# Performance work log

Measured on AMD Instinct MI355X. Metric: run time of the kernel, lower is better.

Reference implementation:

```python
import jax, jax.numpy as jnp
import numpy as np

B, T, H = 64, 256, 768
INIT = 0.05  # keras 'uniform' initializer range


def setup_inputs() -> dict:
    key = jax.random.key(0)
    ks = jax.random.split(key, 11)
    u = lambda k, shape: jax.random.uniform(k, shape, jnp.float32, -INIT, INIT)
    return {
        "q": jax.random.normal(ks[0], (B, T, H), jnp.float32),
        "p": jax.random.normal(ks[1], (B, T, H), jnp.float32),
        "Wc1": u(ks[2], (H, T)),
        "Wc2": u(ks[3], (H, T)),
        "vc": u(ks[4], (T, 1)),
        "Wb": u(ks[5], (H, H)),
        "Wd": u(ks[6], (H, 1)),
        "vd": u(ks[7], (T, 1)),
        "Wm": u(ks[8], (H, 1)),
        "vm": u(ks[9], (T, 1)),
    }


def reference(q, p, Wc1, Wc2, vc, Wb, Wd, vd, Wm, vm):
    # --- additive (concat-style) attention ---
    whq = q @ Wc1                      # [B,T,T]
    whp = p @ Wc2                      # [B,T,T]
    # vc (T,1) broadcasts along axis -2 (the p index i)
    sc = jnp.tanh(whp + jnp.swapaxes(whq, 1, 2)) * vc
    qc = jax.nn.softmax(sc, axis=-1) @ q             # [B,T,H]

    # --- bilinear attention ---
    sb = (p @ Wb) @ jnp.swapaxes(q, 1, 2)            # [B,T,T]
    qb = jax.nn.softmax(sb, axis=-1) @ q

    # --- elementwise-product attention ---
    # sum_h q[b,j,h]*p[b,i,h]*Wd[h]  ==  (p * Wd^T) @ q^T, avoids [B,T,T,H]
    sd_raw = jnp.einsum('bih,bjh->bij', p * Wd[:, 0], q)
    sd = jnp.tanh(sd_raw) * vd[:, 0]                 # vd broadcasts along q index j
    qd = jax.nn.softmax(sd, axis=-1) @ q

    # --- elementwise-difference attention ---
    # sum_h (q[b,j,h]-p[b,i,h])*Wm[h] == (q@Wm)[b,j] - (p@Wm)[b,i]
    qWm = (q @ Wm)[:, :, 0]                          # [B,T]
    pWm = (p @ Wm)[:, :, 0]                          # [B,T]
    sm = jnp.tanh(qWm[:, None, :] - pWm[:, :, None]) * vm[:, 0]
    qm = jax.nn.softmax(sm, axis=-1) @ q

    return (qc, qb, qd, qm)
```

## Files before the change

### kernel.cpp

```cpp
#include <hip/hip_runtime.h>
#include <hip/hip_bf16.h>
#include <stdint.h>

#define NB 64
#define NT 256
#define NH 768

typedef float f32x4 __attribute__((ext_vector_type(4)));
typedef __bf16 bf16x8 __attribute__((ext_vector_type(8)));

static __device__ __forceinline__ uint16_t f2bf(float f) {
  union { float f; uint32_t u; } v; v.f = f;
  uint32_t r = v.u + 0x7FFFu + ((v.u >> 16) & 1u);
  return (uint16_t)(r >> 16);
}
static __device__ __forceinline__ float bf2f(uint16_t h) {
  union { uint32_t u; float f; } v; v.u = ((uint32_t)h) << 16;
  return v.f;
}

typedef const __attribute__((address_space(1))) uint32_t* gp1_t;
typedef __attribute__((address_space(3))) uint32_t* lp3_t;
static __device__ __forceinline__ void gload_lds16(const uint16_t* g, uint16_t* l) {
  __builtin_amdgcn_global_load_lds((gp1_t)g, (lp3_t)l, 16, 0, 0);
}

static __device__ __forceinline__ int xcd_flat(int nwg) {
  int lin = (int)blockIdx.x;
  return (lin & 7) * (nwg >> 3) + (lin >> 3);
}

#define SLOT_U16 16384

static __device__ __forceinline__ void stage_part(
    const uint16_t* __restrict__ Ap, const uint16_t* __restrict__ Bp,
    int k0, int lda, int ldb, int part, uint16_t* __restrict__ slot,
    int wid, int lane) {
  const int isB = part >> 1;
  const int row = (part & 1) * 128 + wid * 16 + (lane >> 2);
  const int kcol = ((lane & 3) * 8) ^ (((lane >> 5) & 1) << 4);
  const uint16_t* src = isB ? Bp + (long)row * ldb + (k0 + kcol)
                            : Ap + (long)row * lda + (k0 + kcol);
  gload_lds16(src, slot + part * 4096 + wid * 512);
}

template <int NPROD, int NKPER>
static __device__ __forceinline__ void gemm256_core(
    const uint16_t* __restrict__ A0, const uint16_t* __restrict__ A1,
    const uint16_t* __restrict__ A2,
    const uint16_t* __restrict__ B0, const uint16_t* __restrict__ B1,
    const uint16_t* __restrict__ B2,
    int lda, int ldb, uint16_t* __restrict__ lds, f32x4 acc[8][4]) {
  const int tid = (int)threadIdx.x;
  const int wid = tid >> 6, lane = tid & 63;
  const int r = lane & 15, quad = lane >> 4;
  const int wm = wid >> 2, wn = wid & 3;
  const int ks = (quad * 8) ^ ((r >> 3) << 4);
  const int abase = (wm * 128 + r) * 32 + ks;
  const int bbase = 8192 + (wn * 64 + r) * 32 + ks;
  constexpr int nk = NPROD * NKPER;

#define TILE_AB(t, Ap, Bp, k0)                                      \
  {                                                                 \
    int pr_ = 0, kk_ = (t);                                         \
    if (NPROD > 1) { pr_ = (t) / NKPER; kk_ = (t) - pr_ * NKPER; }  \
    Ap = pr_ == 0 ? A0 : (pr_ == 1 ? A1 : A2);                      \
    Bp = pr_ == 0 ? B0 : (pr_ == 1 ? B1 : B2);                      \
    k0 = kk_ * 32;                                                  \
  }

  {
    const uint16_t* Ap; const uint16_t* Bp; int k0;
    TILE_AB(0, Ap, Bp, k0);
#pragma unroll
    for (int s = 0; s < 4; ++s) stage_part(Ap, Bp, k0, lda, ldb, s, lds, wid, lane);
    TILE_AB(1, Ap, Bp, k0);
#pragma unroll
    for (int s = 0; s < 4; ++s) stage_part(Ap, Bp, k0, lda, ldb, s, lds + SLOT_U16, wid, lane);
  }

  int slot = 0;
  for (int kt = 0; kt < nk; ++kt) {
    uint16_t* cur = lds + slot * SLOT_U16;
    int ns = slot + 2; if (ns >= 3) ns -= 3;
    uint16_t* nxt = lds + ns * SLOT_U16;
    const uint16_t* An = A0; const uint16_t* Bn = B0; int k0n = 0;
    const bool more2 = (kt + 2 < nk), more1 = (kt + 1 < nk);
    if (more2) TILE_AB(kt + 2, An, Bn, k0n);

#pragma unroll
    for (int p = 0; p < 4; ++p) {
      if (more2) stage_part(An, Bn, k0n, lda, ldb, p, nxt, wid, lane);
      if (p == 0) {
        if (more2)      asm volatile("s_waitcnt vmcnt(5)" ::: "memory");
        else if (more1) asm volatile("s_waitcnt vmcnt(4)" ::: "memory");
        else            asm volatile("s_waitcnt vmcnt(0)" ::: "memory");
        __builtin_amdgcn_s_barrier();
      }
      const int mg = p >> 1, ng = p & 1;
      bf16x8 av[4]; bf16x8 bv[2];
#pragma unroll
      for (int i = 0; i < 4; ++i)
        av[i] = *(const bf16x8*)&cur[abase + (mg * 4 + i) * 512];
#pragma unroll
      for (int j = 0; j < 2; ++j)
        bv[j] = *(const bf16x8*)&cur[bbase + (ng * 2 + j) * 512];
      if (p == 3) {
        asm volatile("s_waitcnt lgkmcnt(0)" ::: "memory");
        __builtin_amdgcn_s_barrier();
      }
      __builtin_amdgcn_s_setprio(1);
#pragma unroll
      for (int i = 0; i < 4; ++i)
#pragma unroll
        for (int j = 0; j < 2; ++j)
          acc[mg * 4 + i][ng * 2 + j] = __builtin_amdgcn_mfma_f32_16x16x32_bf16(
              av[i], bv[j], acc[mg * 4 + i][ng * 2 + j], 0, 0, 0);
      __builtin_amdgcn_s_setprio(0);
    }
    ++slot; if (slot == 3) slot = 0;
  }
#undef TILE_AB
}

static __device__ __forceinline__ void acc_zero8(f32x4 acc[8][4]) {
#pragma unroll
  for (int i = 0; i < 8; ++i)
#pragma unroll
    for (int j = 0; j < 4; ++j) acc[i][j] = (f32x4){0.f, 0.f, 0.f, 0.f};
}

static __device__ __forceinline__ void epi256_f32(const f32x4 acc[8][4],
                                                  float* __restrict__ C, int ldc) {
  const int lane = (int)threadIdx.x & 63, wid = (int)threadIdx.x >> 6;
  const int r = lane & 15, quad = lane >> 4;
  const int wm = wid >> 2, wn = wid & 3;
#pragma unroll
  for (int mi = 0; mi < 8; ++mi) {
    long row = wm * 128 + mi * 16 + quad * 4;
#pragma unroll
    for (int ni = 0; ni < 4; ++ni) {
      long col = wn * 64 + ni * 16 + r;
#pragma unroll
      for (int t = 0; t < 4; ++t) C[(row + t) * ldc + col] = acc[mi][ni][t];
    }
  }
}

static __device__ __forceinline__ void epi256_bf16(const f32x4 acc[8][4],
                                                   uint16_t* __restrict__ C, int ldc) {
  const int lane = (int)threadIdx.x & 63, wid = (int)threadIdx.x >> 6;
  const int r = lane & 15, quad = lane >> 4;
  const int wm = wid >> 2, wn = wid & 3;
#pragma unroll
  for (int mi = 0; mi < 8; ++mi) {
    long row = wm * 128 + mi * 16 + quad * 4;
#pragma unroll
    for (int ni = 0; ni < 4; ++ni) {
      long col = wn * 64 + ni * 16 + r;
#pragma unroll
      for (int t = 0; t < 4; ++t) C[(row + t) * ldc + col] = f2bf(acc[mi][ni][t]);
    }
  }
}

static __device__ __forceinline__ void epi256_split(const f32x4 acc[8][4],
                                                    uint16_t* __restrict__ Ch,
                                                    uint16_t* __restrict__ Cl, int ldc) {
  const int lane = (int)threadIdx.x & 63, wid = (int)threadIdx.x >> 6;
  const int r = lane & 15, quad = lane >> 4;
  const int wm = wid >> 2, wn = wid & 3;
#pragma unroll
  for (int mi = 0; mi < 8; ++mi) {
    long row = wm * 128 + mi * 16 + quad * 4;
#pragma unroll
    for (int ni = 0; ni < 4; ++ni) {
      long col = wn * 64 + ni * 16 + r;
#pragma unroll
      for (int t = 0; t < 4; ++t) {
        float v = acc[mi][ni][t];
        uint16_t hi = f2bf(v);
        Ch[(row + t) * ldc + col] = hi;
        Cl[(row + t) * ldc + col] = f2bf(v - bf2f(hi));
      }
    }
  }
}

__global__ __launch_bounds__(256) void prep_all(
    const float* __restrict__ q, const float* __restrict__ p,
    const float* __restrict__ Wc1, const float* __restrict__ Wc2,
    const float* __restrict__ Wb, const float* __restrict__ Wd,
    const float* __restrict__ Wm,
    uint16_t* __restrict__ q_hi, uint16_t* __restrict__ q_lo,
    uint16_t* __restrict__ p_hi, uint16_t* __restrict__ p_lo,
    uint16_t* __restrict__ pd, uint16_t* __restrict__ qT,
    uint16_t* __restrict__ Wc1T, uint16_t* __restrict__ Wc2T,
    uint16_t* __restrict__ WbTh, uint16_t* __restrict__ WbTl,
    float* __restrict__ qWm, float* __restrict__ pWm) {
  __shared__ float smem[32 * 33];
  const int blk = (int)blockIdx.x;
  const int tid = (int)threadIdx.x;
  if (blk < NB * NT) {
    const long base = (long)blk * NH;
    float sq = 0.f, sp = 0.f;
#pragma unroll
    for (int k = 0; k < 3; ++k) {
      int h = tid + 256 * k;
      long idx = base + h;
      float qv = q[idx], pv = p[idx];
      uint16_t qh = f2bf(qv);
      q_hi[idx] = qh; q_lo[idx] = f2bf(qv - bf2f(qh));
      uint16_t ph = f2bf(pv);
      p_hi[idx] = ph; p_lo[idx] = f2bf(pv - bf2f(ph));
      pd[idx] = f2bf(pv * Wd[h]);
      float w = Wm[h];
      sq += qv * w; sp += pv * w;
    }
    for (int o = 32; o; o >>= 1) { sq += __shfl_down(sq, o); sp += __shfl_down(sp, o); }
    int lane = tid & 63, wv = tid >> 6;
    if (lane == 0) { smem[wv] = sq; smem[4 + wv] = sp; }
    __syncthreads();
    if (tid == 0) {
      qWm[blk] = smem[0] + smem[1] + smem[2] + smem[3];
      pWm[blk] = smem[4] + smem[5] + smem[6] + smem[7];
    }
  } else if (blk < NB * NT + 24 * 8 * NB) {
    int t = blk - NB * NT;
    int ht = t % 24, tt = (t / 24) % 8, b = t / 192;
    int h0 = ht * 32, t0 = tt * 32;
    int tx = tid & 31, ty = tid >> 5;
    const float* src = q + ((long)b * NT + t0) * NH + h0;
    for (int s = 0; s < 32; s += 8) smem[(ty + s) * 33 + tx] = src[(long)(ty + s) * NH + tx];
    __syncthreads();
    uint16_t* dst = qT + ((long)b * NH + h0) * NT + t0;
    for (int s = 0; s < 32; s += 8) dst[(long)(ty + s) * NT + tx] = f2bf(smem[tx * 33 + ty + s]);
  } else {
    int idx = (blk - (NB * NT + 24 * 8 * NB)) * 256 + tid;
    if (idx < NT * NH) {
      int i = idx / NH, h = idx % NH;
      Wc1T[idx] = f2bf(Wc1[h * NT + i]);
      Wc2T[idx] = f2bf(Wc2[h * NT + i]);
    }
    if (idx < NH * NH) {
      int n = idx / NH, k = idx % NH;
      float w = Wb[k * NH + n];
      uint16_t hi = f2bf(w);
      WbTh[idx] = hi;
      WbTl[idx] = f2bf(w - bf2f(hi));
    }
  }
}

__global__ __launch_bounds__(512, 2) void gemm_big3(
    const uint16_t* __restrict__ Wc1T, const uint16_t* __restrict__ Wc2T,
    const uint16_t* __restrict__ q_hi, const uint16_t* __restrict__ p_hi,
    const uint16_t* __restrict__ p_lo, const uint16_t* __restrict__ pd,
    const uint16_t* __restrict__ WbTh, const uint16_t* __restrict__ WbTl,
    uint16_t* __restrict__ whqT, uint16_t* __restrict__ whp,
    uint16_t* __restrict__ sd,
    uint16_t* __restrict__ pWbh, uint16_t* __restrict__ pWbl) {
  __shared__ __align__(16) uint16_t lds[3 * SLOT_U16];
  const long sQP = (long)NT * NH, sTT = (long)NT * NT;
  int w = xcd_flat(384);
  f32x4 acc[8][4];
  acc_zero8(acc);
  if (w < 192) {
    const int b = w / 3, op = w - b * 3;
    const uint16_t* A; const uint16_t* B; uint16_t* C;
    if (op == 0)      { A = Wc1T;           B = q_hi + b * sQP; C = whqT + b * sTT; }
    else if (op == 1) { A = p_hi + b * sQP; B = Wc2T;           C = whp  + b * sTT; }
    else              { A = pd   + b * sQP; B = q_hi + b * sQP; C = sd   + b * sTT; }
    gemm256_core<1, 24>(A, nullptr, nullptr, B, nullptr, nullptr, NH, NH, lds, acc);
    epi256_bf16(acc, C, NT);
  } else {
    const int w2 = w - 192;
    const int b = w2 / 3, nt = w2 - b * 3;
    const uint16_t* Ah = p_hi + b * sQP;
    const uint16_t* Al = p_lo + b * sQP;
    const uint16_t* Bh = WbTh + (long)nt * 256 * NH;
    const uint16_t* Bl = WbTl + (long)nt * 256 * NH;
    gemm256_core<3, 24>(Ah, Ah, Al, Bh, Bl, Bh, NH, NH, lds, acc);
    epi256_split(acc, pWbh + b * sQP + nt * 256, pWbl + b * sQP + nt * 256, NH);
  }
}

__global__ __launch_bounds__(512, 2) void gemm_sb(
    const uint16_t* __restrict__ pWbh, const uint16_t* __restrict__ pWbl,
    const uint16_t* __restrict__ q_hi, const uint16_t* __restrict__ q_lo,
    float* __restrict__ sb0, float* __restrict__ sb1, float* __restrict__ sb2) {
  __shared__ __align__(16) uint16_t lds[3 * SLOT_U16];
  const long sQP = (long)NT * NH, sTT = (long)NT * NT;
  int w = xcd_flat(192);
  const int b = w / 3, pr = w - b * 3;
  const uint16_t* A = (pr == 2 ? pWbl : pWbh) + b * sQP;
  const uint16_t* B = (pr == 1 ? q_lo : q_hi) + b * sQP;
  float* C = (pr == 0 ? sb0 : (pr == 1 ? sb1 : sb2)) + b * sTT;
  f32x4 acc[8][4];
  acc_zero8(acc);
  gemm256_core<1, 24>(A, nullptr, nullptr, B, nullptr, nullptr, NH, NH, lds, acc);
  epi256_f32(acc, C, NT);
}

__global__ __launch_bounds__(512, 2) void gemm_pv(
    const uint16_t* __restrict__ P, const uint16_t* __restrict__ qT,
    float* __restrict__ out) {
  __shared__ __align__(16) uint16_t lds[3 * SLOT_U16];
  const long sQP = (long)NT * NH, sTT = (long)NT * NT;
  const long PB = (long)NB * sTT, nqp = (long)NB * sQP;
  int w = xcd_flat(768);
  const int b = w / 12, rem = w - b * 12;
  const int a = rem >> 2 == 0 ? 0 : rem / 3, nt = rem - (rem / 3) * 3;
  const uint16_t* A = P + (long)(rem / 3) * PB + b * sTT;
  const uint16_t* B = qT + b * sQP + (long)nt * 256 * NT;
  f32x4 acc[8][4];
  acc_zero8(acc);
  gemm256_core<1, 8>(A, nullptr, nullptr, B, nullptr, nullptr, NT, NT, lds, acc);
  (void)a;
  epi256_f32(acc, out + (long)(rem / 3) * nqp + b * sQP + (long)nt * 256, NH);
}

__global__ __launch_bounds__(64) void softmax_k(
    const uint16_t* __restrict__ whp, const uint16_t* __restrict__ whqT,
    const float* __restrict__ sb0, const float* __restrict__ sb1,
    const float* __restrict__ sb2, const uint16_t* __restrict__ sd,
    const float* __restrict__ qWm, const float* __restrict__ pWm,
    const float* __restrict__ vc, const float* __restrict__ vd,
    const float* __restrict__ vm,
    uint16_t* __restrict__ P) {
  int bi = blockIdx.x;
  int b = bi >> 8, i = bi & 255;
  int lane = threadIdx.x;
  long rowoff = (long)bi * NT;
  const long PB = (long)NB * NT * NT;
  float vci = vc[i];
  float pwm = pWm[(long)b * NT + i];
  float vals[4][4];
#pragma unroll
  for (int u = 0; u < 4; ++u) {
    int j = lane + 64 * u;
    long off = rowoff + j;
    vals[0][u] = tanhf(bf2f(whp[off]) + bf2f(whqT[off])) * vci;
    vals[1][u] = sb0[off] + sb1[off] + sb2[off];
    vals[2][u] = tanhf(bf2f(sd[off])) * vd[j];
    vals[3][u] = tanhf(qWm[(long)b * NT + j] - pwm) * vm[j];
  }
#pragma unroll
  for (int a = 0; a < 4; ++a) {
    float m = fmaxf(fmaxf(vals[a][0], vals[a][1]), fmaxf(vals[a][2], vals[a][3]));
    for (int o = 32; o; o >>= 1) m = fmaxf(m, __shfl_xor(m, o));
    float e[4], s = 0.f;
#pragma unroll
    for (int u = 0; u < 4; ++u) { e[u] = __expf(vals[a][u] - m); s += e[u]; }
    for (int o = 32; o; o >>= 1) s += __shfl_xor(s, o);
    float inv = 1.f / s;
#pragma unroll
    for (int u = 0; u < 4; ++u)
      P[a * PB + rowoff + lane + 64 * u] = f2bf(e[u] * inv);
  }
}

extern "C" void kernel_launch(void* const* d_in, const int* in_sizes, int n_in,
                              void* d_out, int out_size, void* d_ws, size_t ws_size,
                              hipStream_t stream) {
  const float* q   = (const float*)d_in[0];
  const float* p   = (const float*)d_in[1];
  const float* Wc1 = (const float*)d_in[2];
  const float* Wc2 = (const float*)d_in[3];
  const float* vc  = (const float*)d_in[4];
  const float* Wb  = (const float*)d_in[5];
  const float* Wd  = (const float*)d_in[6];
  const float* vd  = (const float*)d_in[7];
  const float* Wm  = (const float*)d_in[8];
  const float* vm  = (const float*)d_in[9];
  (void)in_sizes; (void)n_in; (void)out_size; (void)ws_size;

  char* ws = (char*)d_ws;
  size_t o = 0;
  auto alloc = [&](size_t bytes) -> char* {
    char* r = ws + o;
    o = (o + bytes + 255) & ~(size_t)255;
    return r;
  };
  const size_t nqp = (size_t)NB * NT * NH;
  const size_t ntt = (size_t)NB * NT * NT;

  uint16_t* Wc1T = (uint16_t*)alloc((size_t)NT * NH * 2);
  uint16_t* Wc2T = (uint16_t*)alloc((size_t)NT * NH * 2);
  uint16_t* WbTh = (uint16_t*)alloc((size_t)NH * NH * 2);
  uint16_t* WbTl = (uint16_t*)alloc((size_t)NH * NH * 2);
  uint16_t* q_hi = (uint16_t*)alloc(nqp * 2);
  uint16_t* q_lo = (uint16_t*)alloc(nqp * 2);
  uint16_t* p_hi = (uint16_t*)alloc(nqp * 2);
  uint16_t* p_lo = (uint16_t*)alloc(nqp * 2);
  uint16_t* pd   = (uint16_t*)alloc(nqp * 2);
  uint16_t* qT   = (uint16_t*)alloc(nqp * 2);
  float*    qWmB = (float*)alloc((size_t)NB * NT * 4);
  float*    pWmB = (float*)alloc((size_t)NB * NT * 4);
  uint16_t* whp  = (uint16_t*)alloc(ntt * 2);
  uint16_t* whqT = (uint16_t*)alloc(ntt * 2);
  uint16_t* pWbh = (uint16_t*)alloc(nqp * 2);
  uint16_t* pWbl = (uint16_t*)alloc(nqp * 2);
  float*    sb0  = (float*)alloc(ntt * 4);
  uint16_t* sd   = (uint16_t*)alloc(ntt * 2);
  uint16_t* P    = (uint16_t*)alloc(4 * ntt * 2);

  float* sb1 = (float*)p_lo;
  float* sb2 = (float*)pd;

  prep_all<<<dim3(NB * NT + 24 * 8 * NB + (NH * NH + 255) / 256), dim3(256), 0, stream>>>(
      q, p, Wc1, Wc2, Wb, Wd, Wm,
      q_hi, q_lo, p_hi, p_lo, pd, qT, Wc1T, Wc2T, WbTh, WbTl, qWmB, pWmB);

  gemm_big3<<<dim3(384), dim3(512), 0, stream>>>(
      Wc1T, Wc2T, q_hi, p_hi, p_lo, pd, WbTh, WbTl,
      whqT, whp, sd, pWbh, pWbl);

  gemm_sb<<<dim3(192), dim3(512), 0, stream>>>(
      pWbh, pWbl, q_hi, q_lo, sb0, sb1, sb2);

  softmax_k<<<dim3(NB * NT), dim3(64), 0, stream>>>(
      whp, whqT, sb0, sb1, sb2, sd, qWmB, pWmB, vc, vd, vm, P);

  gemm_pv<<<dim3(768), dim3(512), 0, stream>>>(P, qT, (float*)d_out);
}
```

Before: 555.2 us.

## Shrink GEMM tiles to 256x128 with 4 waves and double the grid

All bf16 GEMM kernels switch from 256x256 tiles on 8 waves to 256x128 tiles on 4 waves. The launches double the block count (768, 384 and 1536) to fill the MI355X's CUs better, and block-to-work remapping is updated to match. The inner loop now splits each 32-wide k-step into two MFMA halves, with staging of the next tile interleaved between them. The cost is less operand reuse per tile and different waitcnt and barrier placement. LDS per block also shrinks, which may raise occupancy.

```diff
diff --git a/kernel.cpp b/kernel.cpp
--- a/kernel.cpp
+++ b/kernel.cpp
@@ -25,27 +25,24 @@
   __builtin_amdgcn_global_load_lds((gp1_t)g, (lp3_t)l, 16, 0, 0);
 }
 
-static __device__ __forceinline__ int xcd_flat(int nwg) {
-  int lin = (int)blockIdx.x;
-  return (lin & 7) * (nwg >> 3) + (lin >> 3);
-}
-
-#define SLOT_U16 16384
-
-static __device__ __forceinline__ void stage_part(
+#define SLOT_U16 12288
+
+template <int P0, int P1>
+static __device__ __forceinline__ void stageN(
     const uint16_t* __restrict__ Ap, const uint16_t* __restrict__ Bp,
-    int k0, int lda, int ldb, int part, uint16_t* __restrict__ slot,
-    int wid, int lane) {
-  const int isB = part >> 1;
-  const int row = (part & 1) * 128 + wid * 16 + (lane >> 2);
-  const int kcol = ((lane & 3) * 8) ^ (((lane >> 5) & 1) << 4);
-  const uint16_t* src = isB ? Bp + (long)row * ldb + (k0 + kcol)
-                            : Ap + (long)row * lda + (k0 + kcol);
-  gload_lds16(src, slot + part * 4096 + wid * 512);
+    int k0, int lda, int ldb, uint16_t* __restrict__ slot, int wid, int lane) {
+#pragma unroll
+  for (int part = P0; part < P1; ++part) {
+    const bool isB = part >= 4;
+    const int row = (isB ? (part - 4) : part) * 64 + wid * 16 + (lane >> 2);
+    const int kcol = ((lane & 3) * 8) ^ (((lane >> 5) & 1) << 4);
+    const uint16_t* src = (isB ? Bp + (long)row * ldb : Ap + (long)row * lda) + k0 + kcol;
+    gload_lds16(src, slot + part * 2048 + wid * 512);
+  }
 }
 
 template <int NPROD, int NKPER>
-static __device__ __forceinline__ void gemm256_core(
+static __device__ __forceinline__ void gemm_core(
     const uint16_t* __restrict__ A0, const uint16_t* __restrict__ A1,
     const uint16_t* __restrict__ A2,
     const uint16_t* __restrict__ B0, const uint16_t* __restrict__ B1,
@@ -54,7 +51,7 @@
   const int tid = (int)threadIdx.x;
   const int wid = tid >> 6, lane = tid & 63;
   const int r = lane & 15, quad = lane >> 4;
-  const int wm = wid >> 2, wn = wid & 3;
+  const int wm = wid >> 1, wn = wid & 1;
   const int ks = (quad * 8) ^ ((r >> 3) << 4);
   const int abase = (wm * 128 + r) * 32 + ks;
   const int bbase = 8192 + (wn * 64 + r) * 32 + ks;
@@ -72,11 +69,9 @@
   {
     const uint16_t* Ap; const uint16_t* Bp; int k0;
     TILE_AB(0, Ap, Bp, k0);
-#pragma unroll
-    for (int s = 0; s < 4; ++s) stage_part(Ap, Bp, k0, lda, ldb, s, lds, wid, lane);
+    stageN<0, 6>(Ap, Bp, k0, lda, ldb, lds, wid, lane);
     TILE_AB(1, Ap, Bp, k0);
-#pragma unroll
-    for (int s = 0; s < 4; ++s) stage_part(Ap, Bp, k0, lda, ldb, s, lds + SLOT_U16, wid, lane);
+    stageN<0, 6>(Ap, Bp, k0, lda, ldb, lds + SLOT_U16, wid, lane);
   }
 
   int slot = 0;
@@ -88,36 +83,38 @@
     const bool more2 = (kt + 2 < nk), more1 = (kt + 1 < nk);
     if (more2) TILE_AB(kt + 2, An, Bn, k0n);
 
-#pragma unroll
-    for (int p = 0; p < 4; ++p) {
-      if (more2) stage_part(An, Bn, k0n, lda, ldb, p, nxt, wid, lane);
-      if (p == 0) {
-        if (more2)      asm volatile("s_waitcnt vmcnt(5)" ::: "memory");
-        else if (more1) asm volatile("s_waitcnt vmcnt(4)" ::: "memory");
-        else            asm volatile("s_waitcnt vmcnt(0)" ::: "memory");
-        __builtin_amdgcn_s_barrier();
-      }
-      const int mg = p >> 1, ng = p & 1;
-      bf16x8 av[4]; bf16x8 bv[2];
-#pragma unroll
-      for (int i = 0; i < 4; ++i)
-        av[i] = *(const bf16x8*)&cur[abase + (mg * 4 + i) * 512];
-#pragma unroll
-      for (int j = 0; j < 2; ++j)
-        bv[j] = *(const bf16x8*)&cur[bbase + (ng * 2 + j) * 512];
-      if (p == 3) {
-        asm volatile("s_waitcnt lgkmcnt(0)" ::: "memory");
-        __builtin_amdgcn_s_barrier();
-      }
-      __builtin_amdgcn_s_setprio(1);
-#pragma unroll
-      for (int i = 0; i < 4; ++i)
-#pragma unroll
-        for (int j = 0; j < 2; ++j)
-          acc[mg * 4 + i][ng * 2 + j] = __builtin_amdgcn_mfma_f32_16x16x32_bf16(
-              av[i], bv[j], acc[mg * 4 + i][ng * 2 + j], 0, 0, 0);
-      __builtin_amdgcn_s_setprio(0);
-    }
+    if (more2) stageN<0, 3>(An, Bn, k0n, lda, ldb, nxt, wid, lane);
+    if (more2)      asm volatile("s_waitcnt vmcnt(9)" ::: "memory");
+    else if (more1) asm volatile("s_waitcnt vmcnt(6)" ::: "memory");
+    else            asm volatile("s_waitcnt vmcnt(0)" ::: "memory");
+    __builtin_amdgcn_s_barrier();
+
+    bf16x8 av[4], bv[4];
+#pragma unroll
+    for (int i = 0; i < 4; ++i) av[i] = *(const bf16x8*)&cur[abase + i * 512];
+#pragma unroll
+    for (int j = 0; j < 4; ++j) bv[j] = *(const bf16x8*)&cur[bbase + j * 512];
+    __builtin_amdgcn_s_setprio(1);
+#pragma unroll
+    for (int i = 0; i < 4; ++i)
+#pragma unroll
+      for (int j = 0; j < 4; ++j)
+        acc[i][j] = __builtin_amdgcn_mfma_f32_16x16x32_bf16(av[i], bv[j], acc[i][j], 0, 0, 0);
+    __builtin_amdgcn_s_setprio(0);
+
+    if (more2) stageN<3, 6>(An, Bn, k0n, lda, ldb, nxt, wid, lane);
+#pragma unroll
+    for (int i = 0; i < 4; ++i) av[i] = *(const bf16x8*)&cur[abase + (4 + i) * 512];
+    __builtin_amdgcn_s_setprio(1);
+#pragma unroll
+    for (int i = 0; i < 4; ++i)
+#pragma unroll
+      for (int j = 0; j < 4; ++j)
+        acc[4 + i][j] = __builtin_amdgcn_mfma_f32_16x16x32_bf16(av[i], bv[j], acc[4 + i][j], 0, 0, 0);
+    __builtin_amdgcn_s_setprio(0);
+
+    asm volatile("s_waitcnt lgkmcnt(0)" ::: "memory");
+    __builtin_amdgcn_s_barrier();
     ++slot; if (slot == 3) slot = 0;
   }
 #undef TILE_AB
@@ -130,11 +127,11 @@
     for (int j = 0; j < 4; ++j) acc[i][j] = (f32x4){0.f, 0.f, 0.f, 0.f};
 }
 
-static __device__ __forceinline__ void epi256_f32(const f32x4 acc[8][4],
-                                                  float* __restrict__ C, int ldc) {
+static __device__ __forceinline__ void epi_f32(const f32x4 acc[8][4],
+                                               float* __restrict__ C, int ldc) {
   const int lane = (int)threadIdx.x & 63, wid = (int)threadIdx.x >> 6;
   const int r = lane & 15, quad = lane >> 4;
-  const int wm = wid >> 2, wn = wid & 3;
+  const int wm = wid >> 1, wn = wid & 1;
 #pragma unroll
   for (int mi = 0; mi < 8; ++mi) {
     long row = wm * 128 + mi * 16 + quad * 4;
@@ -147,11 +144,11 @@
   }
 }
 
-static __device__ __forceinline__ void epi256_bf16(const f32x4 acc[8][4],
-                                                   uint16_t* __restrict__ C, int ldc) {
+static __device__ __forceinline__ void epi_bf16(const f32x4 acc[8][4],
+                                                uint16_t* __restrict__ C, int ldc) {
   const int lane = (int)threadIdx.x & 63, wid = (int)threadIdx.x >> 6;
   const int r = lane & 15, quad = lane >> 4;
-  const int wm = wid >> 2, wn = wid & 3;
+  const int wm = wid >> 1, wn = wid & 1;
 #pragma unroll
   for (int mi = 0; mi < 8; ++mi) {
     long row = wm * 128 + mi * 16 + quad * 4;
@@ -164,12 +161,12 @@
   }
 }
 
-static __device__ __forceinline__ void epi256_split(const f32x4 acc[8][4],
-                                                    uint16_t* __restrict__ Ch,
-                                                    uint16_t* __restrict__ Cl, int ldc) {
+static __device__ __forceinline__ void epi_split(const f32x4 acc[8][4],
+                                                 uint16_t* __restrict__ Ch,
+                                                 uint16_t* __restrict__ Cl, int ldc) {
   const int lane = (int)threadIdx.x & 63, wid = (int)threadIdx.x >> 6;
   const int r = lane & 15, quad = lane >> 4;
-  const int wm = wid >> 2, wn = wid & 3;
+  const int wm = wid >> 1, wn = wid & 1;
 #pragma unroll
   for (int mi = 0; mi < 8; ++mi) {
     long row = wm * 128 + mi * 16 + quad * 4;
@@ -252,7 +249,7 @@
   }
 }
 
-__global__ __launch_bounds__(512, 2) void gemm_big3(
+__global__ __launch_bounds__(256, 2) void gemm_big3(
     const uint16_t* __restrict__ Wc1T, const uint16_t* __restrict__ Wc2T,
     const uint16_t* __restrict__ q_hi, const uint16_t* __restrict__ p_hi,
     const uint16_t* __restrict__ p_lo, const uint16_t* __restrict__ pd,
@@ -262,62 +259,67 @@
     uint16_t* __restrict__ pWbh, uint16_t* __restrict__ pWbl) {
   __shared__ __align__(16) uint16_t lds[3 * SLOT_U16];
   const long sQP = (long)NT * NH, sTT = (long)NT * NT;
-  int w = xcd_flat(384);
+  const int bid = (int)blockIdx.x;
   f32x4 acc[8][4];
   acc_zero8(acc);
-  if (w < 192) {
-    const int b = w / 3, op = w - b * 3;
-    const uint16_t* A; const uint16_t* B; uint16_t* C;
-    if (op == 0)      { A = Wc1T;           B = q_hi + b * sQP; C = whqT + b * sTT; }
-    else if (op == 1) { A = p_hi + b * sQP; B = Wc2T;           C = whp  + b * sTT; }
-    else              { A = pd   + b * sQP; B = q_hi + b * sQP; C = sd   + b * sTT; }
-    gemm256_core<1, 24>(A, nullptr, nullptr, B, nullptr, nullptr, NH, NH, lds, acc);
-    epi256_bf16(acc, C, NT);
-  } else {
-    const int w2 = w - 192;
-    const int b = w2 / 3, nt = w2 - b * 3;
+  if (bid < 384) {
+    const int j = (bid & 7) * 48 + (bid >> 3);
+    const int nt = j / 64, b = j - nt * 64;
     const uint16_t* Ah = p_hi + b * sQP;
     const uint16_t* Al = p_lo + b * sQP;
-    const uint16_t* Bh = WbTh + (long)nt * 256 * NH;
-    const uint16_t* Bl = WbTl + (long)nt * 256 * NH;
-    gemm256_core<3, 24>(Ah, Ah, Al, Bh, Bl, Bh, NH, NH, lds, acc);
-    epi256_split(acc, pWbh + b * sQP + nt * 256, pWbl + b * sQP + nt * 256, NH);
-  }
-}
-
-__global__ __launch_bounds__(512, 2) void gemm_sb(
+    const uint16_t* Bh = WbTh + (long)nt * 128 * NH;
+    const uint16_t* Bl = WbTl + (long)nt * 128 * NH;
+    gemm_core<3, 24>(Ah, Ah, Al, Bh, Bl, Bh, NH, NH, lds, acc);
+    epi_split(acc, pWbh + b * sQP + nt * 128, pWbl + b * sQP + nt * 128, NH);
+  } else {
+    const int f = bid - 384;
+    const int j = (f & 7) * 48 + (f >> 3);
+    const int op = j / 128, rem = j - op * 128;
+    const int b = rem >> 1, nh = rem & 1;
+    const uint16_t* A; const uint16_t* B; uint16_t* C;
+    if (op == 0)      { A = Wc1T;           B = q_hi + b * sQP + (long)nh * 128 * NH; C = whqT + b * sTT + nh * 128; }
+    else if (op == 1) { A = p_hi + b * sQP; B = Wc2T + (long)nh * 128 * NH;           C = whp  + b * sTT + nh * 128; }
+    else              { A = pd   + b * sQP; B = q_hi + b * sQP + (long)nh * 128 * NH; C = sd   + b * sTT + nh * 128; }
+    gemm_core<1, 24>(A, nullptr, nullptr, B, nullptr, nullptr, NH, NH, lds, acc);
+    epi_bf16(acc, C, NT);
+  }
+}
+
+__global__ __launch_bounds__(256, 2) void gemm_sb(
     const uint16_t* __restrict__ pWbh, const uint16_t* __restrict__ pWbl,
     const uint16_t* __restrict__ q_hi, const uint16_t* __restrict__ q_lo,
     float* __restrict__ sb0, float* __restrict__ sb1, float* __restrict__ sb2) {
   __shared__ __align__(16) uint16_t lds[3 * SLOT_U16];
   const long sQP = (long)NT * NH, sTT = (long)NT * NT;
-  int w = xcd_flat(192);
-  const int b = w / 3, pr = w - b * 3;
+  const int bid = (int)blockIdx.x;
+  const int j = (bid & 7) * 48 + (bid >> 3);
+  const int pr = j / 128, rem = j - pr * 128;
+  const int b = rem >> 1, nh = rem & 1;
   const uint16_t* A = (pr == 2 ? pWbl : pWbh) + b * sQP;
-  const uint16_t* B = (pr == 1 ? q_lo : q_hi) + b * sQP;
-  float* C = (pr == 0 ? sb0 : (pr == 1 ? sb1 : sb2)) + b * sTT;
+  const uint16_t* B = (pr == 1 ? q_lo : q_hi) + b * sQP + (long)nh * 128 * NH;
+  float* C = (pr == 0 ? sb0 : (pr == 1 ? sb1 : sb2)) + b * sTT + nh * 128;
   f32x4 acc[8][4];
   acc_zero8(acc);
-  gemm256_core<1, 24>(A, nullptr, nullptr, B, nullptr, nullptr, NH, NH, lds, acc);
-  epi256_f32(acc, C, NT);
-}
-
-__global__ __launch_bounds__(512, 2) void gemm_pv(
+  gemm_core<1, 24>(A, nullptr, nullptr, B, nullptr, nullptr, NH, NH, lds, acc);
+  epi_f32(acc, C, NT);
+}
+
+__global__ __launch_bounds__(256, 2) void gemm_pv(
     const uint16_t* __restrict__ P, const uint16_t* __restrict__ qT,
     float* __restrict__ out) {
   __shared__ __align__(16) uint16_t lds[3 * SLOT_U16];
   const long sQP = (long)NT * NH, sTT = (long)NT * NT;
   const long PB = (long)NB * sTT, nqp = (long)NB * sQP;
-  int w = xcd_flat(768);
-  const int b = w / 12, rem = w - b * 12;
-  const int a = rem >> 2 == 0 ? 0 : rem / 3, nt = rem - (rem / 3) * 3;
-  const uint16_t* A = P + (long)(rem / 3) * PB + b * sTT;
-  const uint16_t* B = qT + b * sQP + (long)nt * 256 * NT;
+  const int bid = (int)blockIdx.x;
+  const int j = (bid & 7) * 192 + (bid >> 3);
+  const int a = j / 384, rem = j - a * 384;
+  const int b = rem / 6, nt = rem - b * 6;
+  const uint16_t* A = P + (long)a * PB + b * sTT;
+  const uint16_t* B = qT + b * sQP + (long)nt * 128 * NT;
   f32x4 acc[8][4];
   acc_zero8(acc);
-  gemm256_core<1, 8>(A, nullptr, nullptr, B, nullptr, nullptr, NT, NT, lds, acc);
-  (void)a;
-  epi256_f32(acc, out + (long)(rem / 3) * nqp + b * sQP + (long)nt * 256, NH);
+  gemm_core<1, 8>(A, nullptr, nullptr, B, nullptr, nullptr, NT, NT, lds, acc);
+  epi_f32(acc, out + (long)a * nqp + b * sQP + nt * 128, NH);
 }
 
 __global__ __launch_bounds__(64) void softmax_k(
@@ -412,15 +414,15 @@
       q, p, Wc1, Wc2, Wb, Wd, Wm,
       q_hi, q_lo, p_hi, p_lo, pd, qT, Wc1T, Wc2T, WbTh, WbTl, qWmB, pWmB);
 
-  gemm_big3<<<dim3(384), dim3(512), 0, stream>>>(
+  gemm_big3<<<dim3(768), dim3(256), 0, stream>>>(
       Wc1T, Wc2T, q_hi, p_hi, p_lo, pd, WbTh, WbTl,
       whqT, whp, sd, pWbh, pWbl);
 
-  gemm_sb<<<dim3(192), dim3(512), 0, stream>>>(
+  gemm_sb<<<dim3(384), dim3(256), 0, stream>>>(
       pWbh, pWbl, q_hi, q_lo, sb0, sb1, sb2);
 
   softmax_k<<<dim3(NB * NT), dim3(64), 0, stream>>>(
       whp, whqT, sb0, sb1, sb2, sd, qWmB, pWmB, vc, vd, vm, P);
 
-  gemm_pv<<<dim3(768), dim3(512), 0, stream>>>(P, qT, (float*)d_out);
-}
+  gemm_pv<<<dim3(1536), dim3(256), 0, stream>>>(P, qT, (float*)d_out);
+}
```

After: 543.6 us. 1.02x faster.
